# Optimization experiments

Measured on AMD Instinct MI355X. Metric: run time of the kernel, lower is better.

The kernel has to match this reference:

```python
import jax, jax.numpy as jnp
import numpy as np

N = 50000        # nodes
E = 1600000      # edges (avg degree 32)
F_IN = 512       # input features
HID = 8          # hidden per head (hardcoded in module)
HEADS = 8        # in_head (hardcoded in module)
CLS = 16         # num_classes
NEG_SLOPE = 0.2  # PyG GATConv default


def setup_inputs() -> dict:
    key = jax.random.key(0)
    ks = jax.random.split(key, 12)
    s = 0.05
    return {
        "x": jax.random.normal(ks[0], (N, F_IN), dtype=jnp.float32),
        "edge_index": jax.random.randint(ks[1], (2, E), 0, N, dtype=jnp.int64),
        "W1": jax.random.normal(ks[2], (F_IN, HEADS * HID), dtype=jnp.float32) * s,
        "att_src1": jax.random.normal(ks[3], (HEADS, HID), dtype=jnp.float32) * s,
        "att_dst1": jax.random.normal(ks[4], (HEADS, HID), dtype=jnp.float32) * s,
        "bias1": jax.random.normal(ks[5], (HEADS * HID,), dtype=jnp.float32) * s,
        "W2": jax.random.normal(ks[6], (HEADS * HID, CLS), dtype=jnp.float32) * s,
        "att_src2": jax.random.normal(ks[7], (1, CLS), dtype=jnp.float32) * s,
        "att_dst2": jax.random.normal(ks[8], (1, CLS), dtype=jnp.float32) * s,
        "bias2": jax.random.normal(ks[9], (CLS,), dtype=jnp.float32) * s,
    }


def _gat_conv(x, src, dst, W, att_src, att_dst, bias, n, heads, ch, concat):
    # Linear projection: [n, heads, ch]
    h = (x @ W).reshape(n, heads, ch)
    # Per-node attention logits (PyG style): alpha_src/dst = sum(h * a)
    a_src = jnp.einsum("nhc,hc->nh", h, att_src)  # [n, heads]
    a_dst = jnp.einsum("nhc,hc->nh", h, att_dst)
    # Per-edge raw score, leaky_relu, then segment softmax over incoming edges per dst
    e = jax.nn.leaky_relu(a_src[src] + a_dst[dst], NEG_SLOPE)  # [Etot, heads]
    m = jax.ops.segment_max(e, dst, num_segments=n)            # [n, heads]
    w = jnp.exp(e - m[dst])
    den = jax.ops.segment_sum(w, dst, num_segments=n)
    alpha = w / den[dst]                                        # [Etot, heads]
    # Scatter-aggregate weighted source features
    out = jax.ops.segment_sum(h[src] * alpha[..., None], dst, num_segments=n)  # [n, heads, ch]
    out = out.reshape(n, heads * ch) if concat else out.mean(axis=1)
    return out + bias


def reference(x, edge_index, W1, att_src1, att_dst1, bias1, W2, att_src2, att_dst2, bias2):
    n = x.shape[0]
    # PyG GATConv adds self-loops by default
    loops = jnp.arange(n, dtype=edge_index.dtype)
    src = jnp.concatenate([edge_index[0], loops])
    dst = jnp.concatenate([edge_index[1], loops])
    # dropout(p=0.6) is identity in eval mode
    h = _gat_conv(x, src, dst, W1, att_src1, att_dst1, bias1, n, HEADS, HID, True)
    h = jax.nn.elu(h)
    out = _gat_conv(h, src, dst, W2, att_src2, att_dst2, bias2, n, 1, CLS, False)
    return jax.nn.log_softmax(out, axis=1)
```

## Files before the change

kernel.cpp:

```cpp
#include <hip/hip_runtime.h>
#include <cstddef>

#define N_NODES 50000
#define N_EDGES 1600000
#define N_ETOT  (N_EDGES + N_NODES)
#define F_IN    512
#define HEADS   8
#define HID     8
#define CLS     16

#define NBUCK   196
#define BCAP    12288
#define CHUNKA  4096

typedef float v4 __attribute__((ext_vector_type(4)));
typedef float v2 __attribute__((ext_vector_type(2)));
typedef unsigned short us4 __attribute__((ext_vector_type(4)));
typedef unsigned int u4 __attribute__((ext_vector_type(4)));
typedef short bfrag __attribute__((ext_vector_type(8)));
typedef float ffrag __attribute__((ext_vector_type(4)));

__device__ inline float b2f_lo(unsigned int u) { return __uint_as_float(u << 16); }
__device__ inline float b2f_hi(unsigned int u) { return __uint_as_float(u & 0xffff0000u); }
__device__ inline unsigned short f2b(float f) {
  unsigned int x = __float_as_uint(f);
  unsigned int r = (x + 0x7fffu + ((x >> 16) & 1u)) >> 16;
  return (unsigned short)r;
}

__global__ __launch_bounds__(256) void w1t_kernel(
    const float* __restrict__ W, unsigned short* __restrict__ WT) {
  int t = blockIdx.x * 256 + threadIdx.x;
  if (t >= F_IN * 64) return;
  int k = t >> 6, n = t & 63;
  WT[n * F_IN + k] = f2b(W[t]);
}

__global__ __launch_bounds__(256) void gemm1_kernel(
    const float* __restrict__ x, const unsigned short* __restrict__ W1bT,
    const float* __restrict__ att_src, const float* __restrict__ att_dst,
    unsigned short* __restrict__ h1b, float* __restrict__ a_src,
    float* __restrict__ a_dst, int nrows) {
  __shared__ unsigned short xsb[64][72];
  __shared__ unsigned short wsb[64][72];
  int t = threadIdx.x;
  int lane = t & 63;
  int w = t >> 6;
  int row0 = blockIdx.x * 64;
  ffrag acc[4];
  acc[0] = 0.f; acc[1] = 0.f; acc[2] = 0.f; acc[3] = 0.f;

  int mrow = lane & 15;
  int koff = (lane >> 4) * 8;

  for (int kt = 0; kt < 8; ++kt) {
    int k0 = kt * 64;
#pragma unroll
    for (int r = 0; r < 4; ++r) {
      int slot = t + r * 256;
      int m = slot >> 4;
      int k4 = (slot & 15) * 4;
      v4 v = 0.f;
      int grow = row0 + m;
      if (grow < nrows) v = *(const v4*)(x + (size_t)grow * F_IN + k0 + k4);
      us4 o;
      o.x = f2b(v[0]); o.y = f2b(v[1]); o.z = f2b(v[2]); o.w = f2b(v[3]);
      *(us4*)&xsb[m][k4] = o;
    }
#pragma unroll
    for (int r = 0; r < 2; ++r) {
      int slot = t + r * 256;
      int nn = slot >> 3;
      int k8 = (slot & 7) * 8;
      *(bfrag*)&wsb[nn][k8] = *(const bfrag*)(W1bT + nn * F_IN + k0 + k8);
    }
    __syncthreads();
#pragma unroll
    for (int kk = 0; kk < 64; kk += 32) {
      bfrag a = *(const bfrag*)&xsb[w * 16 + mrow][kk + koff];
#pragma unroll
      for (int tt = 0; tt < 4; ++tt) {
        bfrag b = *(const bfrag*)&wsb[tt * 16 + mrow][kk + koff];
        acc[tt] = __builtin_amdgcn_mfma_f32_16x16x32_bf16(a, b, acc[tt], 0, 0, 0);
      }
    }
    __syncthreads();
  }
  int c = lane & 15, q = lane >> 4;
  float as_[4], ad_[4];
#pragma unroll
  for (int tt = 0; tt < 4; ++tt) {
    as_[tt] = att_src[tt * 16 + c];
    ad_[tt] = att_dst[tt * 16 + c];
  }
#pragma unroll
  for (int r = 0; r < 4; ++r) {
    int grow = row0 + w * 16 + q * 4 + r;
    float ps[4], pd[4];
#pragma unroll
    for (int tt = 0; tt < 4; ++tt) {
      ps[tt] = acc[tt][r] * as_[tt];
      pd[tt] = acc[tt][r] * ad_[tt];
    }
#pragma unroll
    for (int o = 1; o < 8; o <<= 1) {
#pragma unroll
      for (int tt = 0; tt < 4; ++tt) {
        ps[tt] += __shfl_xor(ps[tt], o);
        pd[tt] += __shfl_xor(pd[tt], o);
      }
    }
    if (grow < nrows) {
#pragma unroll
      for (int tt = 0; tt < 4; ++tt)
        h1b[(size_t)grow * 64 + tt * 16 + c] = f2b(acc[tt][r]);
      if ((c & 7) == 0) {
#pragma unroll
        for (int tt = 0; tt < 4; ++tt) {
          int head = tt * 2 + (c >> 3);
          a_src[grow * 8 + head] = ps[tt];
          a_dst[grow * 8 + head] = pd[tt];
        }
      }
    }
  }
}

__global__ __launch_bounds__(256) void bucketA_kernel(
    const int* __restrict__ src_idx, const int* __restrict__ dst_idx,
    int* __restrict__ gcur, int* __restrict__ abuck) {
  __shared__ int hist[NBUCK];
  __shared__ int base[NBUCK];
  __shared__ int cur[NBUCK];
  int t = threadIdx.x;
  if (t < NBUCK) hist[t] = 0;
  __syncthreads();
  int e0 = blockIdx.x * CHUNKA;
  int eend = e0 + CHUNKA;
  if (eend > N_EDGES) eend = N_EDGES;
  for (int e = e0 + t; e < eend; e += 256)
    atomicAdd(&hist[(unsigned)dst_idx[e] >> 8], 1);
  __syncthreads();
  if (t < NBUCK) {
    int c = hist[t];
    base[t] = c ? atomicAdd(&gcur[t], c) : 0;
    cur[t] = 0;
  }
  __syncthreads();
  for (int e = e0 + t; e < eend; e += 256) {
    int s = src_idx[e];
    int d = dst_idx[e];
    int b = (unsigned)d >> 8;
    int r = atomicAdd(&cur[b], 1);
    abuck[b * BCAP + base[b] + r] = (s << 8) | (d & 255);
  }
}

__global__ __launch_bounds__(256) void bucket_scan_kernel(
    const int* __restrict__ gcur, int* __restrict__ bucket_base,
    int* __restrict__ indptr) {
  __shared__ int sm[256];
  int t = threadIdx.x;
  int nnodes = N_NODES - t * 256;
  if (nnodes > 256) nnodes = 256;
  if (nnodes < 0) nnodes = 0;
  int v = (t < NBUCK) ? gcur[t] + nnodes : 0;
  sm[t] = v;
  __syncthreads();
  for (int o = 1; o < 256; o <<= 1) {
    int u = (t >= o) ? sm[t - o] : 0;
    __syncthreads();
    sm[t] += u;
    __syncthreads();
  }
  if (t < NBUCK) bucket_base[t] = sm[t] - v;
  if (t == 0) indptr[N_NODES] = N_ETOT;
}

__global__ __launch_bounds__(256) void bucketB_kernel(
    const int* __restrict__ gcur, const int* __restrict__ bucket_base,
    const int* __restrict__ abuck, int* __restrict__ indptr,
    int* __restrict__ csr_src) {
  __shared__ int hist[256];
  __shared__ int sm[256];
  __shared__ int cur[256];
  int b = blockIdx.x;
  int t = threadIdx.x;
  int M = gcur[b];
  int node0 = b * 256;
  int nnodes = N_NODES - node0;
  if (nnodes > 256) nnodes = 256;
  hist[t] = (t < nnodes) ? 1 : 0;
  __syncthreads();
  const int* ab = abuck + b * BCAP;
  for (int i = t; i < M; i += 256)
    atomicAdd(&hist[ab[i] & 255], 1);
  __syncthreads();
  int v = hist[t];
  sm[t] = v;
  __syncthreads();
  for (int o = 1; o < 256; o <<= 1) {
    int u = (t >= o) ? sm[t - o] : 0;
    __syncthreads();
    sm[t] += u;
    __syncthreads();
  }
  int bbase = bucket_base[b];
  int excl = sm[t] - v;
  cur[t] = excl;
  if (t < nnodes) indptr[node0 + t] = bbase + excl;
  __syncthreads();
  for (int i = t; i < M; i += 256) {
    int entry = ab[i];
    int r = atomicAdd(&cur[entry & 255], 1);
    csr_src[bbase + r] = entry >> 8;
  }
  if (t < nnodes) {
    int r = atomicAdd(&cur[t], 1);
    csr_src[bbase + r] = node0 + t;
  }
}

__global__ __launch_bounds__(256) void agg1_kernel(
    const int* __restrict__ indptr, const int* __restrict__ csr_src,
    const unsigned short* __restrict__ h1b, const float* __restrict__ a_src1,
    const float* __restrict__ a_dst1, const float* __restrict__ bias1,
    float* __restrict__ h_elu, int n) {
  int wave = threadIdx.x >> 6;
  int lane = threadIdx.x & 63;
  int node = blockIdx.x * 4 + wave;
  if (node >= n) return;
  int j = lane >> 3;
  int h = lane & 7;
  float adst = a_dst1[(unsigned)(node * 8 + h)];
  int beg = indptr[node], end = indptr[node + 1];
  float acc0=0.f, acc1=0.f, acc2=0.f, acc3=0.f, acc4=0.f, acc5=0.f, acc6=0.f, acc7=0.f;
  float den = 0.f;
  for (int base = beg; base < end; base += 64) {
    int m = end - base;
    if (m > 64) m = 64;
    int sv = (lane < m) ? csr_src[base + lane] : 0;
    for (int p = 0; p < m; p += 8) {
      int s = __shfl(sv, p + j);
      bool act = (p + j) < m;
      float e = a_src1[(unsigned)(s * 8 + h)] + adst;
      e = (e > 0.f) ? e : 0.2f * e;
      float w = act ? __expf(e) : 0.f;
      den += w;
      u4 f = *(const u4*)(h1b + (unsigned)(s * 64 + h * 8));
      acc0 += w * b2f_lo(f.x); acc1 += w * b2f_hi(f.x);
      acc2 += w * b2f_lo(f.y); acc3 += w * b2f_hi(f.y);
      acc4 += w * b2f_lo(f.z); acc5 += w * b2f_hi(f.z);
      acc6 += w * b2f_lo(f.w); acc7 += w * b2f_hi(f.w);
    }
  }
#pragma unroll
  for (int o = 8; o < 64; o <<= 1) {
    den  += __shfl_xor(den, o);
    acc0 += __shfl_xor(acc0, o); acc1 += __shfl_xor(acc1, o);
    acc2 += __shfl_xor(acc2, o); acc3 += __shfl_xor(acc3, o);
    acc4 += __shfl_xor(acc4, o); acc5 += __shfl_xor(acc5, o);
    acc6 += __shfl_xor(acc6, o); acc7 += __shfl_xor(acc7, o);
  }
  if (j == 0) {
    float inv = 1.f / den;
    v4 b0 = *(const v4*)(bias1 + h * 8);
    v4 b1 = *(const v4*)(bias1 + h * 8 + 4);
    v4 o0, o1;
    o0[0] = acc0 * inv + b0[0]; o0[1] = acc1 * inv + b0[1];
    o0[2] = acc2 * inv + b0[2]; o0[3] = acc3 * inv + b0[3];
    o1[0] = acc4 * inv + b1[0]; o1[1] = acc5 * inv + b1[1];
    o1[2] = acc6 * inv + b1[2]; o1[3] = acc7 * inv + b1[3];
#pragma unroll
    for (int k = 0; k < 4; ++k) {
      o0[k] = (o0[k] > 0.f) ? o0[k] : expm1f(o0[k]);
      o1[k] = (o1[k] > 0.f) ? o1[k] : expm1f(o1[k]);
    }
    *(v4*)(h_elu + (size_t)node * 64 + h * 8)     = o0;
    *(v4*)(h_elu + (size_t)node * 64 + h * 8 + 4) = o1;
  }
}

__global__ __launch_bounds__(256) void gemm2_kernel(
    const float* __restrict__ h_elu, const float* __restrict__ W2,
    const float* __restrict__ att_src2, const float* __restrict__ att_dst2,
    unsigned short* __restrict__ h2b, float* __restrict__ a_src2,
    float* __restrict__ a_dst2, int n) {
  __shared__ float xs[64][68];
  __shared__ float ws[64][16];
  int t = threadIdx.x;
  int row0 = blockIdx.x * 64;
  {
    int k = t >> 2, c4 = (t & 3) * 4;
    *(v4*)&ws[k][c4] = *(const v4*)(W2 + (size_t)k * 16 + c4);
  }
#pragma unroll
  for (int r = 0; r < 4; ++r) {
    int idx = t + r * 256;
    int m = idx >> 4;
    int c4 = (idx & 15) * 4;
    v4 v = 0.f;
    int grow = row0 + m;
    if (grow < n) v = *(const v4*)(h_elu + (size_t)grow * 64 + c4);
    *(v4*)&xs[m][c4] = v;
  }
  __syncthreads();
  int r = t >> 2, q = t & 3;
  int grow = row0 + r;
  v4 acc = 0.f;
#pragma unroll
  for (int k = 0; k < 64; ++k) {
    acc += xs[r][k] * *(const v4*)&ws[k][q * 4];
  }
  v4 asv = *(const v4*)(att_src2 + q * 4);
  v4 adv = *(const v4*)(att_dst2 + q * 4);
  float ps = acc[0] * asv[0] + acc[1] * asv[1] + acc[2] * asv[2] + acc[3] * asv[3];
  float pd = acc[0] * adv[0] + acc[1] * adv[1] + acc[2] * adv[2] + acc[3] * adv[3];
  ps += __shfl_xor(ps, 1); ps += __shfl_xor(ps, 2);
  pd += __shfl_xor(pd, 1); pd += __shfl_xor(pd, 2);
  if (grow < n) {
    us4 o;
    o.x = f2b(acc[0]); o.y = f2b(acc[1]); o.z = f2b(acc[2]); o.w = f2b(acc[3]);
    *(us4*)(h2b + (size_t)grow * 16 + q * 4) = o;
    if (q == 0) { a_src2[grow] = ps; a_dst2[grow] = pd; }
  }
}

__global__ __launch_bounds__(256) void agg2_kernel(
    const int* __restrict__ indptr, const int* __restrict__ csr_src,
    const unsigned short* __restrict__ h2b, const float* __restrict__ a_src2,
    const float* __restrict__ a_dst2, const float* __restrict__ bias2,
    float* __restrict__ out, int n) {
  int wave = threadIdx.x >> 6;
  int lane = threadIdx.x & 63;
  int node = blockIdx.x * 4 + wave;
  if (node >= n) return;
  int j = lane >> 3;
  int sub = lane & 7;
  float adst = a_dst2[node];
  int beg = indptr[node], end = indptr[node + 1];
  float acc0 = 0.f, acc1 = 0.f, den = 0.f;
  for (int base = beg; base < end; base += 64) {
    int m = end - base;
    if (m > 64) m = 64;
    int sv = (lane < m) ? csr_src[base + lane] : 0;
    for (int p = 0; p < m; p += 8) {
      int s = __shfl(sv, p + j);
      bool act = (p + j) < m;
      float e = a_src2[(unsigned)s] + adst;
      e = (e > 0.f) ? e : 0.2f * e;
      float w = act ? __expf(e) : 0.f;
      den += w;
      unsigned int f = *(const unsigned int*)(h2b + (unsigned)(s * 16 + sub * 2));
      acc0 += w * b2f_lo(f);
      acc1 += w * b2f_hi(f);
    }
  }
#pragma unroll
  for (int o = 8; o < 64; o <<= 1) {
    den  += __shfl_xor(den, o);
    acc0 += __shfl_xor(acc0, o);
    acc1 += __shfl_xor(acc1, o);
  }
  float inv = 1.f / den;
  float v0 = acc0 * inv + bias2[sub * 2];
  float v1 = acc1 * inv + bias2[sub * 2 + 1];
  float mx = fmaxf(v0, v1);
#pragma unroll
  for (int o = 1; o < 8; o <<= 1) mx = fmaxf(mx, __shfl_xor(mx, o));
  float ss = __expf(v0 - mx) + __expf(v1 - mx);
#pragma unroll
  for (int o = 1; o < 8; o <<= 1) ss += __shfl_xor(ss, o);
  float lg = mx + __logf(ss);
  if (j == 0) {
    v2 r;
    r[0] = v0 - lg;
    r[1] = v1 - lg;
    *(v2*)(out + (size_t)node * 16 + sub * 2) = r;
  }
}

extern "C" void kernel_launch(void* const* d_in, const int* in_sizes, int n_in,
                              void* d_out, int out_size, void* d_ws, size_t ws_size,
                              hipStream_t stream) {
  const float* x        = (const float*)d_in[0];
  const int*   ei       = (const int*)d_in[1];
  const float* W1       = (const float*)d_in[2];
  const float* att_src1 = (const float*)d_in[3];
  const float* att_dst1 = (const float*)d_in[4];
  const float* bias1    = (const float*)d_in[5];
  const float* W2       = (const float*)d_in[6];
  const float* att_src2 = (const float*)d_in[7];
  const float* att_dst2 = (const float*)d_in[8];
  const float* bias2    = (const float*)d_in[9];
  const int* src_idx = ei;
  const int* dst_idx = ei + N_EDGES;

  char* p = (char*)d_ws;
  auto alloc = [&](size_t bytes) {
    void* r = (void*)p;
    p += (bytes + 255) & ~(size_t)255;
    return r;
  };
  unsigned short* h1b = (unsigned short*)alloc((size_t)N_NODES * 64 * 2);
  float* h_elu   = (float*)alloc((size_t)N_NODES * 64 * 4);
  float* a_src1  = (float*)alloc((size_t)N_NODES * 8 * 4);
  float* a_dst1  = (float*)alloc((size_t)N_NODES * 8 * 4);
  unsigned short* h2b = (unsigned short*)alloc((size_t)N_NODES * 16 * 2);
  float* a_src2  = (float*)alloc((size_t)N_NODES * 4);
  float* a_dst2  = (float*)alloc((size_t)N_NODES * 4);
  int* indptr    = (int*)alloc((size_t)(N_NODES + 1) * 4);
  int* gcur      = (int*)alloc((size_t)NBUCK * 4);
  int* bucket_base = (int*)alloc((size_t)(NBUCK + 1) * 4);
  int* csr_src   = (int*)alloc((size_t)N_ETOT * 4);
  unsigned short* W1bT = (unsigned short*)alloc((size_t)64 * F_IN * 2);
  int* abuck     = (int*)h_elu;

  hipMemsetAsync(gcur, 0, (size_t)NBUCK * 4, stream);

  w1t_kernel<<<(F_IN * 64 + 255) / 256, 256, 0, stream>>>(W1, W1bT);
  gemm1_kernel<<<(N_NODES + 63) / 64, 256, 0, stream>>>(
      x, W1bT, att_src1, att_dst1, h1b, a_src1, a_dst1, N_NODES);

  bucketA_kernel<<<(N_EDGES + CHUNKA - 1) / CHUNKA, 256, 0, stream>>>(
      src_idx, dst_idx, gcur, abuck);
  bucket_scan_kernel<<<1, 256, 0, stream>>>(gcur, bucket_base, indptr);
  bucketB_kernel<<<NBUCK, 256, 0, stream>>>(
      gcur, bucket_base, abuck, indptr, csr_src);

  agg1_kernel<<<N_NODES / 4, 256, 0, stream>>>(
      indptr, csr_src, h1b, a_src1, a_dst1, bias1, h_elu, N_NODES);

  gemm2_kernel<<<(N_NODES + 63) / 64, 256, 0, stream>>>(
      h_elu, W2, att_src2, att_dst2, h2b, a_src2, a_dst2, N_NODES);

  agg2_kernel<<<N_NODES / 4, 256, 0, stream>>>(
      indptr, csr_src, h2b, a_src2, a_dst2, bias2, (float*)d_out, N_NODES);
}
```

Measured before the change: 323.8 us.

## Fuse layer-2 projection into agg1, merge bucket scan, use 16-bit CSR indices

```diff
diff --git a/kernel.cpp b/kernel.cpp
--- a/kernel.cpp
+++ b/kernel.cpp
@@ -29,11 +29,16 @@
 }
 
 __global__ __launch_bounds__(256) void w1t_kernel(
-    const float* __restrict__ W, unsigned short* __restrict__ WT) {
-  int t = blockIdx.x * 256 + threadIdx.x;
-  if (t >= F_IN * 64) return;
-  int k = t >> 6, n = t & 63;
-  WT[n * F_IN + k] = f2b(W[t]);
+    const float* __restrict__ W, unsigned short* __restrict__ WT,
+    int* __restrict__ gcur) {
+  int t = threadIdx.x;
+  if (blockIdx.x == 128) {
+    if (t < NBUCK) gcur[t] = 0;
+    return;
+  }
+  int i = blockIdx.x * 256 + t;
+  int k = i >> 6, n = i & 63;
+  WT[n * F_IN + k] = f2b(W[i]);
 }
 
 __global__ __launch_bounds__(256) void gemm1_kernel(
@@ -156,36 +161,25 @@
   }
 }
 
-__global__ __launch_bounds__(256) void bucket_scan_kernel(
-    const int* __restrict__ gcur, int* __restrict__ bucket_base,
-    int* __restrict__ indptr) {
-  __shared__ int sm[256];
-  int t = threadIdx.x;
-  int nnodes = N_NODES - t * 256;
-  if (nnodes > 256) nnodes = 256;
-  if (nnodes < 0) nnodes = 0;
-  int v = (t < NBUCK) ? gcur[t] + nnodes : 0;
-  sm[t] = v;
-  __syncthreads();
-  for (int o = 1; o < 256; o <<= 1) {
-    int u = (t >= o) ? sm[t - o] : 0;
-    __syncthreads();
-    sm[t] += u;
-    __syncthreads();
-  }
-  if (t < NBUCK) bucket_base[t] = sm[t] - v;
-  if (t == 0) indptr[N_NODES] = N_ETOT;
-}
-
 __global__ __launch_bounds__(256) void bucketB_kernel(
-    const int* __restrict__ gcur, const int* __restrict__ bucket_base,
-    const int* __restrict__ abuck, int* __restrict__ indptr,
-    int* __restrict__ csr_src) {
+    const int* __restrict__ gcur, const int* __restrict__ abuck,
+    int* __restrict__ indptr, unsigned short* __restrict__ csr16) {
+  __shared__ int gs[256];
   __shared__ int hist[256];
   __shared__ int sm[256];
   __shared__ int cur[256];
   int b = blockIdx.x;
   int t = threadIdx.x;
+  int gv = (t < NBUCK) ? gcur[t] : 0;
+  gs[t] = gv;
+  __syncthreads();
+  for (int o = 1; o < 256; o <<= 1) {
+    int u = (t >= o) ? gs[t - o] : 0;
+    __syncthreads();
+    gs[t] += u;
+    __syncthreads();
+  }
+  int bbase = (b > 0 ? gs[b - 1] : 0) + 256 * b;
   int M = gcur[b];
   int node0 = b * 256;
   int nnodes = N_NODES - node0;
@@ -205,27 +199,29 @@
     sm[t] += u;
     __syncthreads();
   }
-  int bbase = bucket_base[b];
   int excl = sm[t] - v;
   cur[t] = excl;
   if (t < nnodes) indptr[node0 + t] = bbase + excl;
+  if (b == NBUCK - 1 && t == 0) indptr[N_NODES] = N_ETOT;
   __syncthreads();
   for (int i = t; i < M; i += 256) {
     int entry = ab[i];
     int r = atomicAdd(&cur[entry & 255], 1);
-    csr_src[bbase + r] = entry >> 8;
+    csr16[bbase + r] = (unsigned short)((unsigned)entry >> 8);
   }
   if (t < nnodes) {
     int r = atomicAdd(&cur[t], 1);
-    csr_src[bbase + r] = node0 + t;
+    csr16[bbase + r] = (unsigned short)(node0 + t);
   }
 }
 
 __global__ __launch_bounds__(256) void agg1_kernel(
-    const int* __restrict__ indptr, const int* __restrict__ csr_src,
+    const int* __restrict__ indptr, const unsigned short* __restrict__ csr16,
     const unsigned short* __restrict__ h1b, const float* __restrict__ a_src1,
     const float* __restrict__ a_dst1, const float* __restrict__ bias1,
-    float* __restrict__ h_elu, int n) {
+    const float* __restrict__ W2, const float* __restrict__ att_src2,
+    const float* __restrict__ att_dst2, unsigned short* __restrict__ h2b,
+    float* __restrict__ a_src2, float* __restrict__ a_dst2, int n) {
   int wave = threadIdx.x >> 6;
   int lane = threadIdx.x & 63;
   int node = blockIdx.x * 4 + wave;
@@ -239,7 +235,7 @@
   for (int base = beg; base < end; base += 64) {
     int m = end - base;
     if (m > 64) m = 64;
-    int sv = (lane < m) ? csr_src[base + lane] : 0;
+    int sv = (lane < m) ? (int)csr16[base + lane] : 0;
     for (int p = 0; p < m; p += 8) {
       int s = __shfl(sv, p + j);
       bool act = (p + j) < m;
@@ -262,72 +258,46 @@
     acc4 += __shfl_xor(acc4, o); acc5 += __shfl_xor(acc5, o);
     acc6 += __shfl_xor(acc6, o); acc7 += __shfl_xor(acc7, o);
   }
-  if (j == 0) {
-    float inv = 1.f / den;
-    v4 b0 = *(const v4*)(bias1 + h * 8);
-    v4 b1 = *(const v4*)(bias1 + h * 8 + 4);
-    v4 o0, o1;
-    o0[0] = acc0 * inv + b0[0]; o0[1] = acc1 * inv + b0[1];
-    o0[2] = acc2 * inv + b0[2]; o0[3] = acc3 * inv + b0[3];
-    o1[0] = acc4 * inv + b1[0]; o1[1] = acc5 * inv + b1[1];
-    o1[2] = acc6 * inv + b1[2]; o1[3] = acc7 * inv + b1[3];
-#pragma unroll
-    for (int k = 0; k < 4; ++k) {
-      o0[k] = (o0[k] > 0.f) ? o0[k] : expm1f(o0[k]);
-      o1[k] = (o1[k] > 0.f) ? o1[k] : expm1f(o1[k]);
-    }
-    *(v4*)(h_elu + (size_t)node * 64 + h * 8)     = o0;
-    *(v4*)(h_elu + (size_t)node * 64 + h * 8 + 4) = o1;
-  }
-}
-
-__global__ __launch_bounds__(256) void gemm2_kernel(
-    const float* __restrict__ h_elu, const float* __restrict__ W2,
-    const float* __restrict__ att_src2, const float* __restrict__ att_dst2,
-    unsigned short* __restrict__ h2b, float* __restrict__ a_src2,
-    float* __restrict__ a_dst2, int n) {
-  __shared__ float xs[64][68];
-  __shared__ float ws[64][16];
-  int t = threadIdx.x;
-  int row0 = blockIdx.x * 64;
-  {
-    int k = t >> 2, c4 = (t & 3) * 4;
-    *(v4*)&ws[k][c4] = *(const v4*)(W2 + (size_t)k * 16 + c4);
-  }
-#pragma unroll
-  for (int r = 0; r < 4; ++r) {
-    int idx = t + r * 256;
-    int m = idx >> 4;
-    int c4 = (idx & 15) * 4;
-    v4 v = 0.f;
-    int grow = row0 + m;
-    if (grow < n) v = *(const v4*)(h_elu + (size_t)grow * 64 + c4);
-    *(v4*)&xs[m][c4] = v;
-  }
-  __syncthreads();
-  int r = t >> 2, q = t & 3;
-  int grow = row0 + r;
-  v4 acc = 0.f;
-#pragma unroll
-  for (int k = 0; k < 64; ++k) {
-    acc += xs[r][k] * *(const v4*)&ws[k][q * 4];
-  }
-  v4 asv = *(const v4*)(att_src2 + q * 4);
-  v4 adv = *(const v4*)(att_dst2 + q * 4);
-  float ps = acc[0] * asv[0] + acc[1] * asv[1] + acc[2] * asv[2] + acc[3] * asv[3];
-  float pd = acc[0] * adv[0] + acc[1] * adv[1] + acc[2] * adv[2] + acc[3] * adv[3];
-  ps += __shfl_xor(ps, 1); ps += __shfl_xor(ps, 2);
-  pd += __shfl_xor(pd, 1); pd += __shfl_xor(pd, 2);
-  if (grow < n) {
-    us4 o;
-    o.x = f2b(acc[0]); o.y = f2b(acc[1]); o.z = f2b(acc[2]); o.w = f2b(acc[3]);
-    *(us4*)(h2b + (size_t)grow * 16 + q * 4) = o;
-    if (q == 0) { a_src2[grow] = ps; a_dst2[grow] = pd; }
-  }
+  float inv = 1.f / den;
+  v4 b0 = *(const v4*)(bias1 + h * 8);
+  v4 b1 = *(const v4*)(bias1 + h * 8 + 4);
+  float oc[8];
+  oc[0] = acc0 * inv + b0[0]; oc[1] = acc1 * inv + b0[1];
+  oc[2] = acc2 * inv + b0[2]; oc[3] = acc3 * inv + b0[3];
+  oc[4] = acc4 * inv + b1[0]; oc[5] = acc5 * inv + b1[1];
+  oc[6] = acc6 * inv + b1[2]; oc[7] = acc7 * inv + b1[3];
+#pragma unroll
+  for (int k = 0; k < 8; ++k)
+    oc[k] = (oc[k] > 0.f) ? oc[k] : expm1f(oc[k]);
+  float p0 = 0.f, p1 = 0.f;
+  const float* w2row = W2 + h * 8 * 16 + 2 * j;
+#pragma unroll
+  for (int k = 0; k < 8; ++k) {
+    v2 wv = *(const v2*)(w2row + k * 16);
+    p0 += oc[k] * wv[0];
+    p1 += oc[k] * wv[1];
+  }
+#pragma unroll
+  for (int o = 1; o < 8; o <<= 1) {
+    p0 += __shfl_xor(p0, o);
+    p1 += __shfl_xor(p1, o);
+  }
+  float ps = p0 * att_src2[2 * j] + p1 * att_src2[2 * j + 1];
+  float pd = p0 * att_dst2[2 * j] + p1 * att_dst2[2 * j + 1];
+#pragma unroll
+  for (int o = 8; o < 64; o <<= 1) {
+    ps += __shfl_xor(ps, o);
+    pd += __shfl_xor(pd, o);
+  }
+  if (h == 0) {
+    unsigned pack = (unsigned)f2b(p0) | ((unsigned)f2b(p1) << 16);
+    *(unsigned*)(h2b + (unsigned)(node * 16 + 2 * j)) = pack;
+  }
+  if (lane == 0) { a_src2[node] = ps; a_dst2[node] = pd; }
 }
 
 __global__ __launch_bounds__(256) void agg2_kernel(
-    const int* __restrict__ indptr, const int* __restrict__ csr_src,
+    const int* __restrict__ indptr, const unsigned short* __restrict__ csr16,
     const unsigned short* __restrict__ h2b, const float* __restrict__ a_src2,
     const float* __restrict__ a_dst2, const float* __restrict__ bias2,
     float* __restrict__ out, int n) {
@@ -343,7 +313,7 @@
   for (int base = beg; base < end; base += 64) {
     int m = end - base;
     if (m > 64) m = 64;
-    int sv = (lane < m) ? csr_src[base + lane] : 0;
+    int sv = (lane < m) ? (int)csr16[base + lane] : 0;
     for (int p = 0; p < m; p += 8) {
       int s = __shfl(sv, p + j);
       bool act = (p + j) < m;
@@ -403,7 +373,6 @@
     return r;
   };
   unsigned short* h1b = (unsigned short*)alloc((size_t)N_NODES * 64 * 2);
-  float* h_elu   = (float*)alloc((size_t)N_NODES * 64 * 4);
   float* a_src1  = (float*)alloc((size_t)N_NODES * 8 * 4);
   float* a_dst1  = (float*)alloc((size_t)N_NODES * 8 * 4);
   unsigned short* h2b = (unsigned short*)alloc((size_t)N_NODES * 16 * 2);
@@ -411,29 +380,22 @@
   float* a_dst2  = (float*)alloc((size_t)N_NODES * 4);
   int* indptr    = (int*)alloc((size_t)(N_NODES + 1) * 4);
   int* gcur      = (int*)alloc((size_t)NBUCK * 4);
-  int* bucket_base = (int*)alloc((size_t)(NBUCK + 1) * 4);
-  int* csr_src   = (int*)alloc((size_t)N_ETOT * 4);
-  unsigned short* W1bT = (unsigned short*)alloc((size_t)64 * F_IN * 2);
-  int* abuck     = (int*)h_elu;
-
-  hipMemsetAsync(gcur, 0, (size_t)NBUCK * 4, stream);
-
-  w1t_kernel<<<(F_IN * 64 + 255) / 256, 256, 0, stream>>>(W1, W1bT);
+  unsigned short* csr16 = (unsigned short*)alloc((size_t)N_ETOT * 2);
+  unsigned short* W1bT  = (unsigned short*)alloc((size_t)64 * F_IN * 2);
+  int* abuck     = (int*)alloc((size_t)NBUCK * BCAP * 4);
+
+  w1t_kernel<<<129, 256, 0, stream>>>(W1, W1bT, gcur);
   gemm1_kernel<<<(N_NODES + 63) / 64, 256, 0, stream>>>(
       x, W1bT, att_src1, att_dst1, h1b, a_src1, a_dst1, N_NODES);
 
   bucketA_kernel<<<(N_EDGES + CHUNKA - 1) / CHUNKA, 256, 0, stream>>>(
       src_idx, dst_idx, gcur, abuck);
-  bucket_scan_kernel<<<1, 256, 0, stream>>>(gcur, bucket_base, indptr);
-  bucketB_kernel<<<NBUCK, 256, 0, stream>>>(
-      gcur, bucket_base, abuck, indptr, csr_src);
+  bucketB_kernel<<<NBUCK, 256, 0, stream>>>(gcur, abuck, indptr, csr16);
 
   agg1_kernel<<<N_NODES / 4, 256, 0, stream>>>(
-      indptr, csr_src, h1b, a_src1, a_dst1, bias1, h_elu, N_NODES);
-
-  gemm2_kernel<<<(N_NODES + 63) / 64, 256, 0, stream>>>(
-      h_elu, W2, att_src2, att_dst2, h2b, a_src2, a_dst2, N_NODES);
+      indptr, csr16, h1b, a_src1, a_dst1, bias1,
+      W2, att_src2, att_dst2, h2b, a_src2, a_dst2, N_NODES);
 
   agg2_kernel<<<N_NODES / 4, 256, 0, stream>>>(
-      indptr, csr_src, h2b, a_src2, a_dst2, bias2, (float*)d_out, N_NODES);
-}
+      indptr, csr16, h2b, a_src2, a_dst2, bias2, (float*)d_out, N_NODES);
+}
```

Result: slower. 341.9 us (+5.6%).

## Shrink CSR indices to 16-bit, merge scan/memset kernels, unroll aggregation loops

Applied to the files above, without the earlier changes.

```diff
diff --git a/kernel.cpp b/kernel.cpp
--- a/kernel.cpp
+++ b/kernel.cpp
@@ -22,6 +22,12 @@
 
 __device__ inline float b2f_lo(unsigned int u) { return __uint_as_float(u << 16); }
 __device__ inline float b2f_hi(unsigned int u) { return __uint_as_float(u & 0xffff0000u); }
+__device__ inline v2 up2(unsigned int u) {
+  v2 r;
+  r[0] = __uint_as_float(u << 16);
+  r[1] = __uint_as_float(u & 0xffff0000u);
+  return r;
+}
 __device__ inline unsigned short f2b(float f) {
   unsigned int x = __float_as_uint(f);
   unsigned int r = (x + 0x7fffu + ((x >> 16) & 1u)) >> 16;
@@ -29,11 +35,16 @@
 }
 
 __global__ __launch_bounds__(256) void w1t_kernel(
-    const float* __restrict__ W, unsigned short* __restrict__ WT) {
-  int t = blockIdx.x * 256 + threadIdx.x;
-  if (t >= F_IN * 64) return;
-  int k = t >> 6, n = t & 63;
-  WT[n * F_IN + k] = f2b(W[t]);
+    const float* __restrict__ W, unsigned short* __restrict__ WT,
+    int* __restrict__ gcur) {
+  int t = threadIdx.x;
+  if (blockIdx.x == 128) {
+    if (t < NBUCK) gcur[t] = 0;
+    return;
+  }
+  int i = blockIdx.x * 256 + t;
+  int k = i >> 6, n = i & 63;
+  WT[n * F_IN + k] = f2b(W[i]);
 }
 
 __global__ __launch_bounds__(256) void gemm1_kernel(
@@ -156,36 +167,25 @@
   }
 }
 
-__global__ __launch_bounds__(256) void bucket_scan_kernel(
-    const int* __restrict__ gcur, int* __restrict__ bucket_base,
-    int* __restrict__ indptr) {
-  __shared__ int sm[256];
-  int t = threadIdx.x;
-  int nnodes = N_NODES - t * 256;
-  if (nnodes > 256) nnodes = 256;
-  if (nnodes < 0) nnodes = 0;
-  int v = (t < NBUCK) ? gcur[t] + nnodes : 0;
-  sm[t] = v;
-  __syncthreads();
-  for (int o = 1; o < 256; o <<= 1) {
-    int u = (t >= o) ? sm[t - o] : 0;
-    __syncthreads();
-    sm[t] += u;
-    __syncthreads();
-  }
-  if (t < NBUCK) bucket_base[t] = sm[t] - v;
-  if (t == 0) indptr[N_NODES] = N_ETOT;
-}
-
 __global__ __launch_bounds__(256) void bucketB_kernel(
-    const int* __restrict__ gcur, const int* __restrict__ bucket_base,
-    const int* __restrict__ abuck, int* __restrict__ indptr,
-    int* __restrict__ csr_src) {
+    const int* __restrict__ gcur, const int* __restrict__ abuck,
+    int* __restrict__ indptr, unsigned short* __restrict__ csr16) {
+  __shared__ int gs[256];
   __shared__ int hist[256];
   __shared__ int sm[256];
   __shared__ int cur[256];
   int b = blockIdx.x;
   int t = threadIdx.x;
+  int gv = (t < NBUCK) ? gcur[t] : 0;
+  gs[t] = gv;
+  __syncthreads();
+  for (int o = 1; o < 256; o <<= 1) {
+    int u = (t >= o) ? gs[t - o] : 0;
+    __syncthreads();
+    gs[t] += u;
+    __syncthreads();
+  }
+  int bbase = (b > 0 ? gs[b - 1] : 0) + 256 * b;
   int M = gcur[b];
   int node0 = b * 256;
   int nnodes = N_NODES - node0;
@@ -205,24 +205,24 @@
     sm[t] += u;
     __syncthreads();
   }
-  int bbase = bucket_base[b];
   int excl = sm[t] - v;
   cur[t] = excl;
   if (t < nnodes) indptr[node0 + t] = bbase + excl;
+  if (b == NBUCK - 1 && t == 0) indptr[N_NODES] = N_ETOT;
   __syncthreads();
   for (int i = t; i < M; i += 256) {
     int entry = ab[i];
     int r = atomicAdd(&cur[entry & 255], 1);
-    csr_src[bbase + r] = entry >> 8;
+    csr16[bbase + r] = (unsigned short)((unsigned)entry >> 8);
   }
   if (t < nnodes) {
     int r = atomicAdd(&cur[t], 1);
-    csr_src[bbase + r] = node0 + t;
+    csr16[bbase + r] = (unsigned short)(node0 + t);
   }
 }
 
 __global__ __launch_bounds__(256) void agg1_kernel(
-    const int* __restrict__ indptr, const int* __restrict__ csr_src,
+    const int* __restrict__ indptr, const unsigned short* __restrict__ csr16,
     const unsigned short* __restrict__ h1b, const float* __restrict__ a_src1,
     const float* __restrict__ a_dst1, const float* __restrict__ bias1,
     float* __restrict__ h_elu, int n) {
@@ -234,47 +234,59 @@
   int h = lane & 7;
   float adst = a_dst1[(unsigned)(node * 8 + h)];
   int beg = indptr[node], end = indptr[node + 1];
-  float acc0=0.f, acc1=0.f, acc2=0.f, acc3=0.f, acc4=0.f, acc5=0.f, acc6=0.f, acc7=0.f;
+  v2 acc[4];
+  acc[0] = 0.f; acc[1] = 0.f; acc[2] = 0.f; acc[3] = 0.f;
   float den = 0.f;
   for (int base = beg; base < end; base += 64) {
     int m = end - base;
     if (m > 64) m = 64;
-    int sv = (lane < m) ? csr_src[base + lane] : 0;
-    for (int p = 0; p < m; p += 8) {
-      int s = __shfl(sv, p + j);
-      bool act = (p + j) < m;
-      float e = a_src1[(unsigned)(s * 8 + h)] + adst;
-      e = (e > 0.f) ? e : 0.2f * e;
-      float w = act ? __expf(e) : 0.f;
-      den += w;
-      u4 f = *(const u4*)(h1b + (unsigned)(s * 64 + h * 8));
-      acc0 += w * b2f_lo(f.x); acc1 += w * b2f_hi(f.x);
-      acc2 += w * b2f_lo(f.y); acc3 += w * b2f_hi(f.y);
-      acc4 += w * b2f_lo(f.z); acc5 += w * b2f_hi(f.z);
-      acc6 += w * b2f_lo(f.w); acc7 += w * b2f_hi(f.w);
+    int sv = (lane < m) ? (int)csr16[base + lane] : 0;
+    for (int p = 0; p < m; p += 16) {
+      int ia = p + j, ib = p + 8 + j;
+      int sa = __shfl(sv, ia & 63);
+      int sb = __shfl(sv, ib & 63);
+      bool aa = ia < m, ab = ib < m;
+      float ga = a_src1[(unsigned)(sa * 8 + h)];
+      float gb = a_src1[(unsigned)(sb * 8 + h)];
+      u4 fa = *(const u4*)(h1b + (unsigned)(sa * 64 + h * 8));
+      u4 fb = *(const u4*)(h1b + (unsigned)(sb * 64 + h * 8));
+      float ea = ga + adst, eb = gb + adst;
+      ea = fmaxf(ea, 0.2f * ea);
+      eb = fmaxf(eb, 0.2f * eb);
+      float wa = aa ? __expf(ea) : 0.f;
+      float wb = ab ? __expf(eb) : 0.f;
+      den += wa + wb;
+      v2 wa2, wb2;
+      wa2[0] = wa; wa2[1] = wa;
+      wb2[0] = wb; wb2[1] = wb;
+      acc[0] += wa2 * up2(fa.x); acc[1] += wa2 * up2(fa.y);
+      acc[2] += wa2 * up2(fa.z); acc[3] += wa2 * up2(fa.w);
+      acc[0] += wb2 * up2(fb.x); acc[1] += wb2 * up2(fb.y);
+      acc[2] += wb2 * up2(fb.z); acc[3] += wb2 * up2(fb.w);
     }
   }
 #pragma unroll
   for (int o = 8; o < 64; o <<= 1) {
-    den  += __shfl_xor(den, o);
-    acc0 += __shfl_xor(acc0, o); acc1 += __shfl_xor(acc1, o);
-    acc2 += __shfl_xor(acc2, o); acc3 += __shfl_xor(acc3, o);
-    acc4 += __shfl_xor(acc4, o); acc5 += __shfl_xor(acc5, o);
-    acc6 += __shfl_xor(acc6, o); acc7 += __shfl_xor(acc7, o);
+    den += __shfl_xor(den, o);
+#pragma unroll
+    for (int i = 0; i < 4; ++i) {
+      acc[i][0] += __shfl_xor(acc[i][0], o);
+      acc[i][1] += __shfl_xor(acc[i][1], o);
+    }
   }
   if (j == 0) {
     float inv = 1.f / den;
     v4 b0 = *(const v4*)(bias1 + h * 8);
     v4 b1 = *(const v4*)(bias1 + h * 8 + 4);
     v4 o0, o1;
-    o0[0] = acc0 * inv + b0[0]; o0[1] = acc1 * inv + b0[1];
-    o0[2] = acc2 * inv + b0[2]; o0[3] = acc3 * inv + b0[3];
-    o1[0] = acc4 * inv + b1[0]; o1[1] = acc5 * inv + b1[1];
-    o1[2] = acc6 * inv + b1[2]; o1[3] = acc7 * inv + b1[3];
+    o0[0] = acc[0][0] * inv + b0[0]; o0[1] = acc[0][1] * inv + b0[1];
+    o0[2] = acc[1][0] * inv + b0[2]; o0[3] = acc[1][1] * inv + b0[3];
+    o1[0] = acc[2][0] * inv + b1[0]; o1[1] = acc[2][1] * inv + b1[1];
+    o1[2] = acc[3][0] * inv + b1[2]; o1[3] = acc[3][1] * inv + b1[3];
 #pragma unroll
     for (int k = 0; k < 4; ++k) {
-      o0[k] = (o0[k] > 0.f) ? o0[k] : expm1f(o0[k]);
-      o1[k] = (o1[k] > 0.f) ? o1[k] : expm1f(o1[k]);
+      o0[k] = (o0[k] > 0.f) ? o0[k] : (__expf(o0[k]) - 1.f);
+      o1[k] = (o1[k] > 0.f) ? o1[k] : (__expf(o1[k]) - 1.f);
     }
     *(v4*)(h_elu + (size_t)node * 64 + h * 8)     = o0;
     *(v4*)(h_elu + (size_t)node * 64 + h * 8 + 4) = o1;
@@ -327,7 +339,7 @@
 }
 
 __global__ __launch_bounds__(256) void agg2_kernel(
-    const int* __restrict__ indptr, const int* __restrict__ csr_src,
+    const int* __restrict__ indptr, const unsigned short* __restrict__ csr16,
     const unsigned short* __restrict__ h2b, const float* __restrict__ a_src2,
     const float* __restrict__ a_dst2, const float* __restrict__ bias2,
     float* __restrict__ out, int n) {
@@ -343,17 +355,24 @@
   for (int base = beg; base < end; base += 64) {
     int m = end - base;
     if (m > 64) m = 64;
-    int sv = (lane < m) ? csr_src[base + lane] : 0;
-    for (int p = 0; p < m; p += 8) {
-      int s = __shfl(sv, p + j);
-      bool act = (p + j) < m;
-      float e = a_src2[(unsigned)s] + adst;
-      e = (e > 0.f) ? e : 0.2f * e;
-      float w = act ? __expf(e) : 0.f;
-      den += w;
-      unsigned int f = *(const unsigned int*)(h2b + (unsigned)(s * 16 + sub * 2));
-      acc0 += w * b2f_lo(f);
-      acc1 += w * b2f_hi(f);
+    int sv = (lane < m) ? (int)csr16[base + lane] : 0;
+    for (int p = 0; p < m; p += 16) {
+      int ia = p + j, ib = p + 8 + j;
+      int sa = __shfl(sv, ia & 63);
+      int sb = __shfl(sv, ib & 63);
+      bool aa = ia < m, ab = ib < m;
+      float ga = a_src2[(unsigned)sa];
+      float gb = a_src2[(unsigned)sb];
+      unsigned fa = *(const unsigned*)(h2b + (unsigned)(sa * 16 + sub * 2));
+      unsigned fb = *(const unsigned*)(h2b + (unsigned)(sb * 16 + sub * 2));
+      float ea = ga + adst, eb = gb + adst;
+      ea = fmaxf(ea, 0.2f * ea);
+      eb = fmaxf(eb, 0.2f * eb);
+      float wa = aa ? __expf(ea) : 0.f;
+      float wb = ab ? __expf(eb) : 0.f;
+      den += wa + wb;
+      acc0 += wa * b2f_lo(fa) + wb * b2f_lo(fb);
+      acc1 += wa * b2f_hi(fa) + wb * b2f_hi(fb);
     }
   }
 #pragma unroll
@@ -411,29 +430,24 @@
   float* a_dst2  = (float*)alloc((size_t)N_NODES * 4);
   int* indptr    = (int*)alloc((size_t)(N_NODES + 1) * 4);
   int* gcur      = (int*)alloc((size_t)NBUCK * 4);
-  int* bucket_base = (int*)alloc((size_t)(NBUCK + 1) * 4);
-  int* csr_src   = (int*)alloc((size_t)N_ETOT * 4);
-  unsigned short* W1bT = (unsigned short*)alloc((size_t)64 * F_IN * 2);
+  unsigned short* csr16 = (unsigned short*)alloc((size_t)N_ETOT * 2);
+  unsigned short* W1bT  = (unsigned short*)alloc((size_t)64 * F_IN * 2);
   int* abuck     = (int*)h_elu;
 
-  hipMemsetAsync(gcur, 0, (size_t)NBUCK * 4, stream);
-
-  w1t_kernel<<<(F_IN * 64 + 255) / 256, 256, 0, stream>>>(W1, W1bT);
+  w1t_kernel<<<129, 256, 0, stream>>>(W1, W1bT, gcur);
   gemm1_kernel<<<(N_NODES + 63) / 64, 256, 0, stream>>>(
       x, W1bT, att_src1, att_dst1, h1b, a_src1, a_dst1, N_NODES);
 
   bucketA_kernel<<<(N_EDGES + CHUNKA - 1) / CHUNKA, 256, 0, stream>>>(
       src_idx, dst_idx, gcur, abuck);
-  bucket_scan_kernel<<<1, 256, 0, stream>>>(gcur, bucket_base, indptr);
-  bucketB_kernel<<<NBUCK, 256, 0, stream>>>(
-      gcur, bucket_base, abuck, indptr, csr_src);
+  bucketB_kernel<<<NBUCK, 256, 0, stream>>>(gcur, abuck, indptr, csr16);
 
   agg1_kernel<<<N_NODES / 4, 256, 0, stream>>>(
-      indptr, csr_src, h1b, a_src1, a_dst1, bias1, h_elu, N_NODES);
+      indptr, csr16, h1b, a_src1, a_dst1, bias1, h_elu, N_NODES);
 
   gemm2_kernel<<<(N_NODES + 63) / 64, 256, 0, stream>>>(
       h_elu, W2, att_src2, att_dst2, h2b, a_src2, a_dst2, N_NODES);
 
   agg2_kernel<<<N_NODES / 4, 256, 0, stream>>>(
-      indptr, csr_src, h2b, a_src2, a_dst2, bias2, (float*)d_out, N_NODES);
-}
+      indptr, csr16, h2b, a_src2, a_dst2, bias2, (float*)d_out, N_NODES);
+}
```

After: 296.8 us. -8.3%, faster.
